# Optimization experiments

Measured on AMD Instinct MI355X. Metric: run time of the kernel, lower is better.

## Reference

```python
import jax, jax.numpy as jnp
import numpy as np

NEG_SLOPE = 0.2


def gat_layer(x, src, dst, W, a_src, a_dst, b, heads, out_c, concat):
    N = x.shape[0]
    h = (x @ W).reshape(N, heads, out_c)                      # [N,H,C]
    alpha_s = jnp.einsum('nhc,hc->nh', h, a_src)              # [N,H]
    alpha_d = jnp.einsum('nhc,hc->nh', h, a_dst)              # [N,H]
    e = jax.nn.leaky_relu(alpha_s[src] + alpha_d[dst], NEG_SLOPE)  # [E,H]
    # softmax over incoming edges per destination node (segment softmax)
    m = jax.ops.segment_max(e, dst, num_segments=N)
    m = jnp.where(jnp.isfinite(m), m, 0.0)
    ex = jnp.exp(e - m[dst])
    denom = jax.ops.segment_sum(ex, dst, num_segments=N)
    alpha = ex / (denom[dst] + 1e-16)                         # [E,H]
    out = jax.ops.segment_sum(alpha[:, :, None] * h[src], dst, num_segments=N)  # [N,H,C]
    out = out.reshape(N, heads * out_c) if concat else out.mean(axis=1)
    return out + b


def setup_inputs() -> dict:
    key = jax.random.key(0)
    ks = jax.random.split(key, 12)
    N, E, D, H, C, G = 20000, 160000, 256, 4, 128, 64
    x = jax.random.normal(ks[0], (N, D), dtype=jnp.float32)
    edge_index = jax.random.randint(ks[1], (2, E), 0, N)
    batch = jnp.sort(jax.random.randint(ks[2], (N,), 0, G))
    s = 0.05
    params = {
        'W1': jax.random.normal(ks[3], (D, H * C), jnp.float32) * s,
        'a_src1': jax.random.normal(ks[4], (H, C), jnp.float32) * s,
        'a_dst1': jax.random.normal(ks[5], (H, C), jnp.float32) * s,
        'b1': jnp.zeros((H * C,), jnp.float32),
        'W2': jax.random.normal(ks[6], (H * C, C), jnp.float32) * s,
        'a_src2': jax.random.normal(ks[7], (1, C), jnp.float32) * s,
        'a_dst2': jax.random.normal(ks[8], (1, C), jnp.float32) * s,
        'b2': jnp.zeros((C,), jnp.float32),
        'fc1_W': jax.random.normal(ks[9], (C, C // 2), jnp.float32) * s,
        'fc1_b': jnp.zeros((C // 2,), jnp.float32),
        'fc2_W': jax.random.normal(ks[10], (C // 2, 1), jnp.float32) * s,
        'fc2_b': jnp.zeros((1,), jnp.float32),
    }
    return dict(x=x, edge_index=edge_index, batch=batch, **params)


def reference(x, edge_index, batch, W1, a_src1, a_dst1, b1, W2, a_src2, a_dst2, b2,
              fc1_W, fc1_b, fc2_W, fc2_b):
    N = x.shape[0]
    G = 64  # number of graphs
    # add self-loops (PyG GATConv default)
    loop = jnp.arange(N, dtype=edge_index.dtype)
    src = jnp.concatenate([edge_index[0], loop])
    dst = jnp.concatenate([edge_index[1], loop])
    h = jax.nn.relu(gat_layer(x, src, dst, W1, a_src1, a_dst1, b1, 4, 128, True))
    h = gat_layer(h, src, dst, W2, a_src2, a_dst2, b2, 1, 128, False)
    # global mean pool per graph
    sums = jax.ops.segment_sum(h, batch, num_segments=G)
    cnts = jax.ops.segment_sum(jnp.ones((N,), h.dtype), batch, num_segments=G)
    pooled = sums / jnp.maximum(cnts, 1.0)[:, None]          # [G,128]
    out = jax.nn.relu(pooled @ fc1_W + fc1_b)
    return out @ fc2_W + fc2_b                                # [G,1]
```

## Files before the change

### kernel.cpp

```cpp
#include <hip/hip_runtime.h>
#include <hip/hip_bf16.h>
#include <cstdint>
#include <cstddef>

#define NEG_SLOPE 0.2f

typedef __attribute__((ext_vector_type(8))) __bf16 bf16x8;
typedef __attribute__((ext_vector_type(4))) __bf16 bf16x4;
typedef __attribute__((ext_vector_type(2))) __bf16 bf16x2;
typedef __attribute__((ext_vector_type(4))) float  f32x4;

__device__ __forceinline__ float lrelu(float v) {
    return (v < 0.f) ? NEG_SLOPE * v : v;
}

template<int MF, int NF, bool STORE_BF16>
__global__ __launch_bounds__(256) void gemm_mfma(
    const __bf16* __restrict__ A, const __bf16* __restrict__ Bt,
    void* __restrict__ Cout, int M, int N, int K)
{
    const int tid  = threadIdx.x;
    const int wave = tid >> 6, lane = tid & 63;
    const int wr = wave >> 1, wc = wave & 1;
    const int rowbase = blockIdx.y * (32 * MF) + wr * (16 * MF);
    const int colbase = blockIdx.x * (32 * NF) + wc * (16 * NF);
    const int l15 = lane & 15, kg = lane >> 4;

    size_t aoff[MF], boff[NF];
    #pragma unroll
    for (int mf = 0; mf < MF; ++mf) {
        int r = rowbase + mf * 16 + l15;
        if (r > M - 1) r = M - 1;
        aoff[mf] = (size_t)r * K + kg * 8;
    }
    #pragma unroll
    for (int nf = 0; nf < NF; ++nf) {
        int c = colbase + nf * 16 + l15;
        boff[nf] = (size_t)c * K + kg * 8;
    }

    f32x4 acc[MF][NF];
    #pragma unroll
    for (int mf = 0; mf < MF; ++mf)
        #pragma unroll
        for (int nf = 0; nf < NF; ++nf)
            acc[mf][nf] = (f32x4){0.f, 0.f, 0.f, 0.f};

    #pragma unroll 2
    for (int k0 = 0; k0 < K; k0 += 32) {
        bf16x8 af[MF], bfr[NF];
        #pragma unroll
        for (int mf = 0; mf < MF; ++mf)
            af[mf] = *(const bf16x8*)(A + aoff[mf] + k0);
        #pragma unroll
        for (int nf = 0; nf < NF; ++nf)
            bfr[nf] = *(const bf16x8*)(Bt + boff[nf] + k0);
        #pragma unroll
        for (int mf = 0; mf < MF; ++mf)
            #pragma unroll
            for (int nf = 0; nf < NF; ++nf)
                acc[mf][nf] = __builtin_amdgcn_mfma_f32_16x16x32_bf16(af[mf], bfr[nf], acc[mf][nf], 0, 0, 0);
    }

    #pragma unroll
    for (int mf = 0; mf < MF; ++mf)
        #pragma unroll
        for (int j = 0; j < 4; ++j) {
            int r = rowbase + mf * 16 + kg * 4 + j;
            if (r < M) {
                #pragma unroll
                for (int nf = 0; nf < NF; ++nf) {
                    int c = colbase + nf * 16 + l15;
                    if (STORE_BF16)
                        ((__bf16*)Cout)[(size_t)r * N + c] = (__bf16)acc[mf][nf][j];
                    else
                        ((float*)Cout)[(size_t)r * N + c] = acc[mf][nf][j];
                }
            }
        }
}

__global__ __launch_bounds__(256) void gemm1_agg(
    const __bf16* __restrict__ aggx,
    const __bf16* __restrict__ w1t,
    const float* __restrict__ b1, const float* __restrict__ wsd2,
    __bf16* __restrict__ out1b,
    float* __restrict__ ps_part, float* __restrict__ pd_part,
    int M)
{
    const int head = blockIdx.x;
    const int tid  = threadIdx.x;
    const int wave = tid >> 6, lane = tid & 63;
    const int wr = wave >> 1, wc = wave & 1;
    const int rowbase = blockIdx.y * 128 + wr * 64;
    const int l15 = lane & 15, kg = lane >> 4;

    size_t aoff[4], boff[4];
    #pragma unroll
    for (int mf = 0; mf < 4; ++mf) {
        int r = rowbase + mf * 16 + l15;
        if (r > M - 1) r = M - 1;
        aoff[mf] = (size_t)r * 1024 + head * 256 + kg * 8;
    }
    #pragma unroll
    for (int nf = 0; nf < 4; ++nf) {
        int c = head * 128 + wc * 64 + nf * 16 + l15;
        boff[nf] = (size_t)c * 256 + kg * 8;
    }

    f32x4 acc[4][4];
    #pragma unroll
    for (int mf = 0; mf < 4; ++mf)
        #pragma unroll
        for (int nf = 0; nf < 4; ++nf)
            acc[mf][nf] = (f32x4){0.f, 0.f, 0.f, 0.f};

    #pragma unroll 2
    for (int k0 = 0; k0 < 256; k0 += 32) {
        bf16x8 af[4], bfr[4];
        #pragma unroll
        for (int mf = 0; mf < 4; ++mf)
            af[mf] = *(const bf16x8*)(aggx + aoff[mf] + k0);
        #pragma unroll
        for (int nf = 0; nf < 4; ++nf)
            bfr[nf] = *(const bf16x8*)(w1t + boff[nf] + k0);
        #pragma unroll
        for (int mf = 0; mf < 4; ++mf)
            #pragma unroll
            for (int nf = 0; nf < 4; ++nf)
                acc[mf][nf] = __builtin_amdgcn_mfma_f32_16x16x32_bf16(af[mf], bfr[nf], acc[mf][nf], 0, 0, 0);
    }

    __shared__ float smp[2][128], smd[2][128];

    #pragma unroll
    for (int mf = 0; mf < 4; ++mf)
        #pragma unroll
        for (int j = 0; j < 4; ++j) {
            int r = rowbase + mf * 16 + kg * 4 + j;
            float ps = 0.f, pd = 0.f;
            #pragma unroll
            for (int nf = 0; nf < 4; ++nf) {
                int col = head * 128 + wc * 64 + nf * 16 + l15;
                float o = fmaxf(acc[mf][nf][j] + b1[col], 0.f);
                if (r < M)
                    out1b[(size_t)r * 512 + col] = (__bf16)o;
                ps = fmaf(o, wsd2[col], ps);
                pd = fmaf(o, wsd2[512 + col], pd);
            }
            #pragma unroll
            for (int t = 1; t < 16; t <<= 1) {
                ps += __shfl_xor(ps, t);
                pd += __shfl_xor(pd, t);
            }
            if (l15 == 0) {
                int lr = wr * 64 + mf * 16 + kg * 4 + j;
                smp[wc][lr] = ps;
                smd[wc][lr] = pd;
            }
        }
    __syncthreads();
    if (tid < 128) {
        int r = blockIdx.y * 128 + tid;
        if (r < M) {
            ps_part[(size_t)r * 4 + head] = smp[0][tid] + smp[1][tid];
            pd_part[(size_t)r * 4 + head] = smd[0][tid] + smd[1][tid];
        }
    }
}

__global__ void prep_kernel(const float* __restrict__ W1, const float* __restrict__ W2,
                            const float* __restrict__ as1w, const float* __restrict__ ad1w,
                            const float* __restrict__ as2w, const float* __restrict__ ad2w,
                            const int* __restrict__ batch,
                            __bf16* __restrict__ w1t, __bf16* __restrict__ w2t,
                            float* __restrict__ wsd1, float* __restrict__ wsd2,
                            int* __restrict__ gstart, int* __restrict__ cnt,
                            int N, int G)
{
    int t = blockIdx.x * 256 + threadIdx.x;
    if (t < 131072) {
        int i = t;
        int k = i >> 9, n = i & 511;
        w1t[n * 256 + k] = (__bf16)W1[i];
    } else if (t < 196608) {
        int j = t - 131072;
        int k = j >> 7, n = j & 127;
        w2t[n * 512 + k] = (__bf16)W2[j];
    } else if (t < 199680) {
        int t2 = t - 196608;
        if (t2 < 2048) {
            int k = t2 >> 3, v = t2 & 7, h = v >> 1;
            const float* av = (v & 1) ? (ad1w + h * 128) : (as1w + h * 128);
            float s = 0.f;
            for (int c = 0; c < 128; ++c) s += W1[k * 512 + h * 128 + c] * av[c];
            wsd1[v * 256 + k] = s;
        } else {
            int t3 = t2 - 2048;
            int k = t3 >> 1, v = t3 & 1;
            const float* av = v ? ad2w : as2w;
            float s = 0.f;
            for (int c = 0; c < 128; ++c) s += W2[k * 128 + c] * av[c];
            wsd2[v * 512 + k] = s;
        }
    } else if (t < 199680 + N) {
        int n = t - 199680;
        int b    = batch[n];
        int prev = (n == 0) ? -1 : batch[n - 1];
        for (int g = prev + 1; g <= b; ++g) gstart[g] = n;
        if (n == N - 1) {
            for (int g = b + 1; g <= G; ++g) gstart[g] = N;
        }
    } else if (t < 199680 + 2 * N) {
        cnt[t - 199680 - N] = 0;
    }
}

__global__ __launch_bounds__(256) void count_cvtx(
    const int* __restrict__ ei, int* __restrict__ cnt,
    const float* __restrict__ x, const float* __restrict__ wsd1,
    __bf16* __restrict__ xb, float* __restrict__ as1_, float* __restrict__ ad1_,
    int ET, int E0, int N, int CB)
{
    if ((int)blockIdx.x < CB) {
        int e = blockIdx.x * 256 + threadIdx.x;
        if (e >= ET) return;
        int d = (e < E0) ? ei[E0 + e] : (e - E0);
        atomicAdd(&cnt[d], 1);
        return;
    }
    int bid = blockIdx.x - CB;
    int wave = threadIdx.x >> 6, lane = threadIdx.x & 63;
    int n = bid * 4 + wave;
    if (n >= N) return;
    float4 xv = *(const float4*)&x[(size_t)n * 256 + lane * 4];
    bf16x4 xo;
    xo[0] = (__bf16)xv.x; xo[1] = (__bf16)xv.y; xo[2] = (__bf16)xv.z; xo[3] = (__bf16)xv.w;
    *(bf16x4*)&xb[(size_t)n * 256 + lane * 4] = xo;
    float p[8];
    #pragma unroll
    for (int v = 0; v < 8; ++v) {
        float4 wv = *(const float4*)&wsd1[v * 256 + lane * 4];
        p[v] = xv.x * wv.x + xv.y * wv.y + xv.z * wv.z + xv.w * wv.w;
    }
    #pragma unroll
    for (int v = 0; v < 8; ++v)
        #pragma unroll
        for (int s = 1; s < 64; s <<= 1) p[v] += __shfl_xor(p[v], s);
    if (lane == 0) {
        #pragma unroll
        for (int h = 0; h < 4; ++h) {
            as1_[n * 4 + h] = p[2 * h];
            ad1_[n * 4 + h] = p[2 * h + 1];
        }
    }
}

__global__ __launch_bounds__(1024) void scan_gmax(
    const int* __restrict__ cnt, int* __restrict__ offs, int* __restrict__ cur,
    const float* __restrict__ as1_, float* __restrict__ gmax1, int n)
{
    constexpr int CHUNK = 20;
    int t = threadIdx.x;
    int base = t * CHUNK;
    int v[CHUNK];
    int s = 0;
    #pragma unroll
    for (int i = 0; i < CHUNK; ++i) {
        int idx = base + i;
        int xv = (idx < n) ? cnt[idx] : 0;
        v[i] = s; s += xv;
    }
    int lane = t & 63, w = t >> 6;
    int sc = s;
    #pragma unroll
    for (int d = 1; d < 64; d <<= 1) {
        int o = __shfl_up(sc, d);
        if (lane >= d) sc += o;
    }
    __shared__ int wt[16], wb[17];
    __shared__ float gsm[16][4];
    if (lane == 63) wt[w] = sc;
    __syncthreads();
    if (t == 0) {
        int acc = 0;
        for (int i = 0; i < 16; ++i) { wb[i] = acc; acc += wt[i]; }
        wb[16] = acc;
    }
    __syncthreads();
    int ebase = wb[w] + (sc - s);
    #pragma unroll
    for (int i = 0; i < CHUNK; ++i) {
        int idx = base + i;
        if (idx < n) {
            int o = ebase + v[i];
            offs[idx] = o;
            cur[idx]  = o;
        }
    }
    if (t == 0) offs[n] = wb[16];

    float lm0 = -1e30f, lm1 = -1e30f, lm2 = -1e30f, lm3 = -1e30f;
    for (int i = t; i < n; i += 1024) {
        float4 a = *(const float4*)&as1_[(size_t)i * 4];
        lm0 = fmaxf(lm0, a.x); lm1 = fmaxf(lm1, a.y);
        lm2 = fmaxf(lm2, a.z); lm3 = fmaxf(lm3, a.w);
    }
    #pragma unroll
    for (int d = 1; d < 64; d <<= 1) {
        lm0 = fmaxf(lm0, __shfl_xor(lm0, d));
        lm1 = fmaxf(lm1, __shfl_xor(lm1, d));
        lm2 = fmaxf(lm2, __shfl_xor(lm2, d));
        lm3 = fmaxf(lm3, __shfl_xor(lm3, d));
    }
    if (lane == 0) {
        gsm[w][0] = lm0; gsm[w][1] = lm1; gsm[w][2] = lm2; gsm[w][3] = lm3;
    }
    __syncthreads();
    if (t == 0) {
        float m0 = -1e30f, m1 = -1e30f, m2 = -1e30f, m3 = -1e30f;
        for (int i = 0; i < 16; ++i) {
            m0 = fmaxf(m0, gsm[i][0]); m1 = fmaxf(m1, gsm[i][1]);
            m2 = fmaxf(m2, gsm[i][2]); m3 = fmaxf(m3, gsm[i][3]);
        }
        gmax1[0] = m0; gmax1[1] = m1; gmax1[2] = m2; gmax1[3] = m3;
    }
}

__global__ void scatter_kernel(const int* __restrict__ ei, int* __restrict__ cur,
                               int* __restrict__ eid, int ET, int E0)
{
    int e = blockIdx.x * blockDim.x + threadIdx.x;
    if (e >= ET) return;
    int d   = (e < E0) ? ei[E0 + e] : (e - E0);
    int pos = atomicAdd(&cur[d], 1);
    eid[pos] = e;
}

__global__ __launch_bounds__(256) void aggx_kernel(
    const __bf16* __restrict__ xb, const int* __restrict__ offs,
    const int* __restrict__ eid, const int* __restrict__ ei,
    const float* __restrict__ as1_, const float* __restrict__ ad1_,
    const float* __restrict__ gmax1,
    __bf16* __restrict__ aggx, int E0, int N)
{
    int wave = threadIdx.x >> 6, lane = threadIdx.x & 63;
    int n = blockIdx.x * 4 + wave;
    if (n >= N) return;
    int s0 = offs[n], s1 = offs[n + 1];
    float4 adv = *(const float4*)&ad1_[(size_t)n * 4];
    float m0 = lrelu(gmax1[0] + adv.x);
    float m1 = lrelu(gmax1[1] + adv.y);
    float m2 = lrelu(gmax1[2] + adv.z);
    float m3 = lrelu(gmax1[3] + adv.w);

    float d0 = 0.f, d1 = 0.f, d2 = 0.f, d3 = 0.f;
    float a0[4] = {0.f,0.f,0.f,0.f}, a1[4] = {0.f,0.f,0.f,0.f};
    float a2[4] = {0.f,0.f,0.f,0.f}, a3[4] = {0.f,0.f,0.f,0.f};
    const __bf16* xbase = xb + lane * 4;

    int j = s0;
    for (; j + 7 < s1; j += 8) {
        int s_[8]; float4 av_[8]; bf16x4 xv_[8];
        #pragma unroll
        for (int i = 0; i < 8; ++i) {
            int e = eid[j + i];
            s_[i] = (e < E0) ? ei[e] : (e - E0);
        }
        #pragma unroll
        for (int i = 0; i < 8; ++i) av_[i] = *(const float4*)&as1_[(size_t)s_[i] * 4];
        #pragma unroll
        for (int i = 0; i < 8; ++i) xv_[i] = *(const bf16x4*)(xbase + (size_t)s_[i] * 256);
        #pragma unroll
        for (int i = 0; i < 8; ++i) {
            float w0 = __expf(lrelu(av_[i].x + adv.x) - m0); d0 += w0;
            float w1 = __expf(lrelu(av_[i].y + adv.y) - m1); d1 += w1;
            float w2 = __expf(lrelu(av_[i].z + adv.z) - m2); d2 += w2;
            float w3 = __expf(lrelu(av_[i].w + adv.w) - m3); d3 += w3;
            float xf[4];
            #pragma unroll
            for (int c = 0; c < 4; ++c) xf[c] = (float)xv_[i][c];
            #pragma unroll
            for (int c = 0; c < 4; ++c) {
                a0[c] = fmaf(w0, xf[c], a0[c]);
                a1[c] = fmaf(w1, xf[c], a1[c]);
                a2[c] = fmaf(w2, xf[c], a2[c]);
                a3[c] = fmaf(w3, xf[c], a3[c]);
            }
        }
    }
    for (; j < s1; ++j) {
        int e = eid[j];
        int s = (e < E0) ? ei[e] : (e - E0);
        float4 av = *(const float4*)&as1_[(size_t)s * 4];
        bf16x4 xv = *(const bf16x4*)(xbase + (size_t)s * 256);
        float w0 = __expf(lrelu(av.x + adv.x) - m0); d0 += w0;
        float w1 = __expf(lrelu(av.y + adv.y) - m1); d1 += w1;
        float w2 = __expf(lrelu(av.z + adv.z) - m2); d2 += w2;
        float w3 = __expf(lrelu(av.w + adv.w) - m3); d3 += w3;
        float xf[4];
        #pragma unroll
        for (int c = 0; c < 4; ++c) xf[c] = (float)xv[c];
        #pragma unroll
        for (int c = 0; c < 4; ++c) {
            a0[c] = fmaf(w0, xf[c], a0[c]);
            a1[c] = fmaf(w1, xf[c], a1[c]);
            a2[c] = fmaf(w2, xf[c], a2[c]);
            a3[c] = fmaf(w3, xf[c], a3[c]);
        }
    }

    float i0 = 1.f / (d0 + 1e-16f);
    float i1 = 1.f / (d1 + 1e-16f);
    float i2 = 1.f / (d2 + 1e-16f);
    float i3 = 1.f / (d3 + 1e-16f);
    __bf16* obase = aggx + (size_t)n * 1024 + lane * 4;
    bf16x4 o;
    #pragma unroll
    for (int c = 0; c < 4; ++c) o[c] = (__bf16)(a0[c] * i0);
    *(bf16x4*)(obase + 0)   = o;
    #pragma unroll
    for (int c = 0; c < 4; ++c) o[c] = (__bf16)(a1[c] * i1);
    *(bf16x4*)(obase + 256) = o;
    #pragma unroll
    for (int c = 0; c < 4; ++c) o[c] = (__bf16)(a2[c] * i2);
    *(bf16x4*)(obase + 512) = o;
    #pragma unroll
    for (int c = 0; c < 4; ++c) o[c] = (__bf16)(a3[c] * i3);
    *(bf16x4*)(obase + 768) = o;
}

__global__ __launch_bounds__(256) void aggregate2_kernel(
    const __bf16* __restrict__ h2b, const int* __restrict__ offs,
    const int* __restrict__ eid, const int* __restrict__ ei,
    const float* __restrict__ ps_part, const float* __restrict__ pd_part,
    const float* __restrict__ b2, float* __restrict__ out2, int E0, int N)
{
    int wave = threadIdx.x >> 6, lane = threadIdx.x & 63;
    int n = blockIdx.x * 4 + wave;
    if (n >= N) return;
    int s0 = offs[n], s1 = offs[n + 1];
    float4 pdv = *(const float4*)&pd_part[(size_t)n * 4];
    float adn = (pdv.x + pdv.y) + (pdv.z + pdv.w);

    float m = -1e30f;
    for (int j = s0 + lane; j < s1; j += 64) {
        int e = eid[j];
        int s = (e < E0) ? ei[e] : (e - E0);
        float4 pv = *(const float4*)&ps_part[(size_t)s * 4];
        float v = lrelu(((pv.x + pv.y) + (pv.z + pv.w)) + adn);
        m = fmaxf(m, v);
    }
    #pragma unroll
    for (int t = 1; t < 64; t <<= 1) m = fmaxf(m, __shfl_xor(m, t));

    float den = 0.f;
    float c0 = 0.f, c1 = 0.f;
    const __bf16* hbase = h2b + lane * 2;
    int j = s0;
    for (; j + 7 < s1; j += 8) {
        int s_[8]; float4 pv_[8]; bf16x2 h_[8];
        #pragma unroll
        for (int i = 0; i < 8; ++i) {
            int e = eid[j + i];
            s_[i] = (e < E0) ? ei[e] : (e - E0);
        }
        #pragma unroll
        for (int i = 0; i < 8; ++i) pv_[i] = *(const float4*)&ps_part[(size_t)s_[i] * 4];
        #pragma unroll
        for (int i = 0; i < 8; ++i) h_[i] = *(const bf16x2*)(hbase + (size_t)s_[i] * 128);
        #pragma unroll
        for (int i = 0; i < 8; ++i) {
            float v = lrelu(((pv_[i].x + pv_[i].y) + (pv_[i].z + pv_[i].w)) + adn);
            float w = __expf(v - m);
            den += w;
            c0 = fmaf(w, (float)h_[i][0], c0);
            c1 = fmaf(w, (float)h_[i][1], c1);
        }
    }
    for (; j < s1; ++j) {
        int e = eid[j];
        int s = (e < E0) ? ei[e] : (e - E0);
        float4 pv = *(const float4*)&ps_part[(size_t)s * 4];
        float v = lrelu(((pv.x + pv.y) + (pv.z + pv.w)) + adn);
        float w = __expf(v - m);
        den += w;
        bf16x2 hv = *(const bf16x2*)(hbase + (size_t)s * 128);
        c0 = fmaf(w, (float)hv[0], c0);
        c1 = fmaf(w, (float)hv[1], c1);
    }
    float inv = 1.f / (den + 1e-16f);
    float2 o;
    o.x = c0 * inv + b2[lane * 2 + 0];
    o.y = c1 * inv + b2[lane * 2 + 1];
    *(float2*)&out2[(size_t)n * 128 + lane * 2] = o;
}

#define POOL_S 16
__global__ void pool_stage1(const float* __restrict__ out2, const int* __restrict__ gstart,
                            float* __restrict__ partial, int C)
{
    int g = blockIdx.x, slice = blockIdx.y;
    int c = threadIdx.x;
    int s = gstart[g], e = gstart[g + 1];
    int len = e - s;
    int chunk = (len + POOL_S - 1) / POOL_S;
    int n0 = s + slice * chunk;
    int n1 = min(n0 + chunk, e);
    float acc = 0.f;
    for (int n = n0; n < n1; ++n) acc += out2[(size_t)n * C + c];
    partial[((size_t)g * POOL_S + slice) * C + c] = acc;
}

__global__ __launch_bounds__(128) void pool_head(
    const float* __restrict__ partial, const int* __restrict__ gstart,
    const float* __restrict__ fc1W, const float* __restrict__ fc1b,
    const float* __restrict__ fc2W, const float* __restrict__ fc2b,
    float* __restrict__ out)
{
    int g = blockIdx.x;
    int t = threadIdx.x;
    __shared__ float pl[128];
    float acc = 0.f;
    #pragma unroll
    for (int s = 0; s < POOL_S; ++s)
        acc += partial[((size_t)g * POOL_S + s) * 128 + t];
    float cntf = (float)(gstart[g + 1] - gstart[g]);
    pl[t] = acc / fmaxf(cntf, 1.0f);
    __syncthreads();
    if (t < 64) {
        float v = 0.f;
        for (int c = 0; c < 128; ++c)
            v += pl[c] * fc1W[c * 64 + t];
        v = fmaxf(v + fc1b[t], 0.f) * fc2W[t];
        #pragma unroll
        for (int s = 32; s > 0; s >>= 1) v += __shfl_down(v, s);
        if (t == 0) out[g] = v + fc2b[0];
    }
}

extern "C" void kernel_launch(void* const* d_in, const int* in_sizes, int n_in,
                              void* d_out, int out_size, void* d_ws, size_t ws_size,
                              hipStream_t stream)
{
    const float* x    = (const float*)d_in[0];
    const int*   ei   = (const int*)d_in[1];
    const int*   batch= (const int*)d_in[2];
    const float* W1   = (const float*)d_in[3];
    const float* as1w = (const float*)d_in[4];
    const float* ad1w = (const float*)d_in[5];
    const float* b1   = (const float*)d_in[6];
    const float* W2   = (const float*)d_in[7];
    const float* as2w = (const float*)d_in[8];
    const float* ad2w = (const float*)d_in[9];
    const float* b2   = (const float*)d_in[10];
    const float* fc1W = (const float*)d_in[11];
    const float* fc1b = (const float*)d_in[12];
    const float* fc2W = (const float*)d_in[13];
    const float* fc2b = (const float*)d_in[14];
    float* out = (float*)d_out;

    const int D = 256, C = 128, G = 64;
    const int N  = in_sizes[0] / D;
    const int E0 = in_sizes[1] / 2;
    const int ET = E0 + N;

    char* p = (char*)d_ws;
    auto alloc = [&](size_t bytes) -> char* {
        char* r = p;
        p += (bytes + 255) & ~(size_t)255;
        return r;
    };
    __bf16* xb    = (__bf16*)alloc((size_t)N * D * 2);
    __bf16* aggx  = (__bf16*)alloc((size_t)N * 4 * 256 * 2);
    __bf16* out1b = (__bf16*)alloc((size_t)N * 512 * 2);
    __bf16* h2b   = (__bf16*)alloc((size_t)N * C * 2);
    float*  out2  = (float*)alloc((size_t)N * C * 4);
    __bf16* w1t   = (__bf16*)alloc((size_t)256 * 512 * 2);
    __bf16* w2t   = (__bf16*)alloc((size_t)512 * 128 * 2);
    float* wsd1   = (float*)alloc(8 * 256 * 4);
    float* wsd2   = (float*)alloc(2 * 512 * 4);
    float* gmax1  = (float*)alloc(4 * 4);
    float* as1_   = (float*)alloc((size_t)N * 4 * 4);
    float* ad1_   = (float*)alloc((size_t)N * 4 * 4);
    float* ps_part= (float*)alloc((size_t)N * 4 * 4);
    float* pd_part= (float*)alloc((size_t)N * 4 * 4);
    int*   cnt    = (int*)alloc((size_t)N * 4);
    int*   cur    = (int*)alloc((size_t)N * 4);
    int*   offs   = (int*)alloc((size_t)(N + 1) * 4);
    int*   eid    = (int*)alloc((size_t)ET * 4);
    int*   gstart = (int*)alloc((size_t)(G + 1) * 4);
    float* partial= (float*)alloc((size_t)G * POOL_S * C * 4);

    {
        int total = 199680 + 2 * N;
        prep_kernel<<<(total + 255) / 256, 256, 0, stream>>>(
            W1, W2, as1w, ad1w, as2w, ad2w, batch,
            w1t, w2t, wsd1, wsd2, gstart, cnt, N, G);
    }

    {
        int CB = (ET + 255) / 256;
        count_cvtx<<<CB + N / 4, 256, 0, stream>>>(
            ei, cnt, x, wsd1, xb, as1_, ad1_, ET, E0, N, CB);
    }

    scan_gmax<<<1, 1024, 0, stream>>>(cnt, offs, cur, as1_, gmax1, N);

    scatter_kernel<<<(ET + 255) / 256, 256, 0, stream>>>(ei, cur, eid, ET, E0);

    aggx_kernel<<<(N + 3) / 4, 256, 0, stream>>>(
        xb, offs, eid, ei, as1_, ad1_, gmax1, aggx, E0, N);

    gemm1_agg<<<dim3(4, (N + 127) / 128), 256, 0, stream>>>(
        aggx, w1t, b1, wsd2, out1b, ps_part, pd_part, N);

    gemm_mfma<2, 2, true><<<dim3(C / 64, (N + 63) / 64), 256, 0, stream>>>(
        out1b, w2t, h2b, N, C, 512);

    aggregate2_kernel<<<(N + 3) / 4, 256, 0, stream>>>(
        h2b, offs, eid, ei, ps_part, pd_part, b2, out2, E0, N);

    pool_stage1<<<dim3(G, POOL_S), C, 0, stream>>>(out2, gstart, partial, C);
    pool_head<<<G, 128, 0, stream>>>(partial, gstart, fc1W, fc1b, fc2W, fc2b, out);
}
```

Before: 222.1 us.

## Store source ids in CSR, precompute per-edge weights cooperatively, use global-max softmax bound

The scatter kernel now stores source node ids directly, which removes the eid-to-ei indirection in both aggregation kernels. In each aggregation, every lane computes one edge's softmax weight at once and stages it in shared memory, so weights are no longer recomputed redundantly by all 64 lanes. Layer 2 drops its per-node max pass in favour of a global max of alpha_src, found by a new kernel with an ordered-key atomicMax, plus precomputed scalar as2/ad2 arrays. A global upper bound for the shift risks exp underflow when scores are widely spread, and the shared memory is reused across chunks without an explicit wave barrier.

```diff
diff --git a/kernel.cpp b/kernel.cpp
--- a/kernel.cpp
+++ b/kernel.cpp
@@ -12,6 +12,15 @@
 
 __device__ __forceinline__ float lrelu(float v) {
     return (v < 0.f) ? NEG_SLOPE * v : v;
+}
+
+__device__ __forceinline__ unsigned fkey(float x) {
+    unsigned b = __float_as_uint(x);
+    return b ^ (unsigned)(((int)b >> 31) | 0x80000000);
+}
+__device__ __forceinline__ float funkey(unsigned k) {
+    unsigned b = (k & 0x80000000u) ? (k ^ 0x80000000u) : ~k;
+    return __uint_as_float(b);
 }
 
 template<int MF, int NF, bool STORE_BF16>
@@ -176,6 +185,7 @@
                             __bf16* __restrict__ w1t, __bf16* __restrict__ w2t,
                             float* __restrict__ wsd1, float* __restrict__ wsd2,
                             int* __restrict__ gstart, int* __restrict__ cnt,
+                            unsigned* __restrict__ gmax2u,
                             int N, int G)
 {
     int t = blockIdx.x * 256 + threadIdx.x;
@@ -213,6 +223,8 @@
         }
     } else if (t < 199680 + 2 * N) {
         cnt[t - 199680 - N] = 0;
+    } else if (t == 199680 + 2 * N) {
+        *gmax2u = fkey(-1e30f);
     }
 }
 
@@ -328,22 +340,25 @@
 }
 
 __global__ void scatter_kernel(const int* __restrict__ ei, int* __restrict__ cur,
-                               int* __restrict__ eid, int ET, int E0)
+                               int* __restrict__ srcs, int ET, int E0)
 {
     int e = blockIdx.x * blockDim.x + threadIdx.x;
     if (e >= ET) return;
-    int d   = (e < E0) ? ei[E0 + e] : (e - E0);
+    int d = (e < E0) ? ei[E0 + e] : (e - E0);
+    int s = (e < E0) ? ei[e] : (e - E0);
     int pos = atomicAdd(&cur[d], 1);
-    eid[pos] = e;
+    srcs[pos] = s;
 }
 
 __global__ __launch_bounds__(256) void aggx_kernel(
     const __bf16* __restrict__ xb, const int* __restrict__ offs,
-    const int* __restrict__ eid, const int* __restrict__ ei,
+    const int* __restrict__ srcs,
     const float* __restrict__ as1_, const float* __restrict__ ad1_,
     const float* __restrict__ gmax1,
-    __bf16* __restrict__ aggx, int E0, int N)
-{
+    __bf16* __restrict__ aggx, int N)
+{
+    __shared__ float w4s[4][64][4];
+    __shared__ int   sidx[4][64];
     int wave = threadIdx.x >> 6, lane = threadIdx.x & 63;
     int n = blockIdx.x * 4 + wave;
     if (n >= N) return;
@@ -359,55 +374,68 @@
     float a2[4] = {0.f,0.f,0.f,0.f}, a3[4] = {0.f,0.f,0.f,0.f};
     const __bf16* xbase = xb + lane * 4;
 
-    int j = s0;
-    for (; j + 7 < s1; j += 8) {
-        int s_[8]; float4 av_[8]; bf16x4 xv_[8];
-        #pragma unroll
-        for (int i = 0; i < 8; ++i) {
-            int e = eid[j + i];
-            s_[i] = (e < E0) ? ei[e] : (e - E0);
-        }
-        #pragma unroll
-        for (int i = 0; i < 8; ++i) av_[i] = *(const float4*)&as1_[(size_t)s_[i] * 4];
-        #pragma unroll
-        for (int i = 0; i < 8; ++i) xv_[i] = *(const bf16x4*)(xbase + (size_t)s_[i] * 256);
-        #pragma unroll
-        for (int i = 0; i < 8; ++i) {
-            float w0 = __expf(lrelu(av_[i].x + adv.x) - m0); d0 += w0;
-            float w1 = __expf(lrelu(av_[i].y + adv.y) - m1); d1 += w1;
-            float w2 = __expf(lrelu(av_[i].z + adv.z) - m2); d2 += w2;
-            float w3 = __expf(lrelu(av_[i].w + adv.w) - m3); d3 += w3;
+    for (int base = s0; base < s1; base += 64) {
+        int cnt = min(64, s1 - base);
+        if (lane < cnt) {
+            int s = srcs[base + lane];
+            float4 av = *(const float4*)&as1_[(size_t)s * 4];
+            float w0 = __expf(lrelu(av.x + adv.x) - m0);
+            float w1 = __expf(lrelu(av.y + adv.y) - m1);
+            float w2 = __expf(lrelu(av.z + adv.z) - m2);
+            float w3 = __expf(lrelu(av.w + adv.w) - m3);
+            d0 += w0; d1 += w1; d2 += w2; d3 += w3;
+            sidx[wave][lane] = s;
+            w4s[wave][lane][0] = w0; w4s[wave][lane][1] = w1;
+            w4s[wave][lane][2] = w2; w4s[wave][lane][3] = w3;
+        }
+        int j = 0;
+        for (; j + 7 < cnt; j += 8) {
+            int s_[8]; float4 w_[8]; bf16x4 xv_[8];
+            #pragma unroll
+            for (int i = 0; i < 8; ++i) {
+                s_[i] = sidx[wave][j + i];
+                w_[i] = *(const float4*)&w4s[wave][j + i][0];
+            }
+            #pragma unroll
+            for (int i = 0; i < 8; ++i)
+                xv_[i] = *(const bf16x4*)(xbase + (size_t)s_[i] * 256);
+            #pragma unroll
+            for (int i = 0; i < 8; ++i) {
+                float xf[4];
+                #pragma unroll
+                for (int c = 0; c < 4; ++c) xf[c] = (float)xv_[i][c];
+                #pragma unroll
+                for (int c = 0; c < 4; ++c) {
+                    a0[c] = fmaf(w_[i].x, xf[c], a0[c]);
+                    a1[c] = fmaf(w_[i].y, xf[c], a1[c]);
+                    a2[c] = fmaf(w_[i].z, xf[c], a2[c]);
+                    a3[c] = fmaf(w_[i].w, xf[c], a3[c]);
+                }
+            }
+        }
+        for (; j < cnt; ++j) {
+            int s = sidx[wave][j];
+            float4 w = *(const float4*)&w4s[wave][j][0];
+            bf16x4 xv = *(const bf16x4*)(xbase + (size_t)s * 256);
             float xf[4];
             #pragma unroll
-            for (int c = 0; c < 4; ++c) xf[c] = (float)xv_[i][c];
+            for (int c = 0; c < 4; ++c) xf[c] = (float)xv[c];
             #pragma unroll
             for (int c = 0; c < 4; ++c) {
-                a0[c] = fmaf(w0, xf[c], a0[c]);
-                a1[c] = fmaf(w1, xf[c], a1[c]);
-                a2[c] = fmaf(w2, xf[c], a2[c]);
-                a3[c] = fmaf(w3, xf[c], a3[c]);
-            }
-        }
-    }
-    for (; j < s1; ++j) {
-        int e = eid[j];
-        int s = (e < E0) ? ei[e] : (e - E0);
-        float4 av = *(const float4*)&as1_[(size_t)s * 4];
-        bf16x4 xv = *(const bf16x4*)(xbase + (size_t)s * 256);
-        float w0 = __expf(lrelu(av.x + adv.x) - m0); d0 += w0;
-        float w1 = __expf(lrelu(av.y + adv.y) - m1); d1 += w1;
-        float w2 = __expf(lrelu(av.z + adv.z) - m2); d2 += w2;
-        float w3 = __expf(lrelu(av.w + adv.w) - m3); d3 += w3;
-        float xf[4];
-        #pragma unroll
-        for (int c = 0; c < 4; ++c) xf[c] = (float)xv[c];
-        #pragma unroll
-        for (int c = 0; c < 4; ++c) {
-            a0[c] = fmaf(w0, xf[c], a0[c]);
-            a1[c] = fmaf(w1, xf[c], a1[c]);
-            a2[c] = fmaf(w2, xf[c], a2[c]);
-            a3[c] = fmaf(w3, xf[c], a3[c]);
-        }
+                a0[c] = fmaf(w.x, xf[c], a0[c]);
+                a1[c] = fmaf(w.y, xf[c], a1[c]);
+                a2[c] = fmaf(w.z, xf[c], a2[c]);
+                a3[c] = fmaf(w.w, xf[c], a3[c]);
+            }
+        }
+    }
+
+    #pragma unroll
+    for (int t = 1; t < 64; t <<= 1) {
+        d0 += __shfl_xor(d0, t);
+        d1 += __shfl_xor(d1, t);
+        d2 += __shfl_xor(d2, t);
+        d3 += __shfl_xor(d3, t);
     }
 
     float i0 = 1.f / (d0 + 1e-16f);
@@ -430,65 +458,84 @@
     *(bf16x4*)(obase + 768) = o;
 }
 
+__global__ __launch_bounds__(256) void sum2_kernel(
+    const float* __restrict__ ps_part, const float* __restrict__ pd_part,
+    float* __restrict__ as2, float* __restrict__ ad2,
+    unsigned* __restrict__ gmax2u, int N)
+{
+    int i = blockIdx.x * 256 + threadIdx.x;
+    float lm = -1e30f;
+    if (i < N) {
+        float4 p = *(const float4*)&ps_part[(size_t)i * 4];
+        float4 q = *(const float4*)&pd_part[(size_t)i * 4];
+        float s = (p.x + p.y) + (p.z + p.w);
+        float d = (q.x + q.y) + (q.z + q.w);
+        as2[i] = s;
+        ad2[i] = d;
+        lm = s;
+    }
+    #pragma unroll
+    for (int t = 1; t < 64; t <<= 1) lm = fmaxf(lm, __shfl_xor(lm, t));
+    if ((threadIdx.x & 63) == 0) atomicMax(gmax2u, fkey(lm));
+}
+
 __global__ __launch_bounds__(256) void aggregate2_kernel(
     const __bf16* __restrict__ h2b, const int* __restrict__ offs,
-    const int* __restrict__ eid, const int* __restrict__ ei,
-    const float* __restrict__ ps_part, const float* __restrict__ pd_part,
-    const float* __restrict__ b2, float* __restrict__ out2, int E0, int N)
-{
+    const int* __restrict__ srcs,
+    const float* __restrict__ as2, const float* __restrict__ ad2,
+    const unsigned* __restrict__ gmax2u,
+    const float* __restrict__ b2, float* __restrict__ out2, int N)
+{
+    __shared__ float wls[4][64];
+    __shared__ int   sidx[4][64];
     int wave = threadIdx.x >> 6, lane = threadIdx.x & 63;
     int n = blockIdx.x * 4 + wave;
     if (n >= N) return;
     int s0 = offs[n], s1 = offs[n + 1];
-    float4 pdv = *(const float4*)&pd_part[(size_t)n * 4];
-    float adn = (pdv.x + pdv.y) + (pdv.z + pdv.w);
-
-    float m = -1e30f;
-    for (int j = s0 + lane; j < s1; j += 64) {
-        int e = eid[j];
-        int s = (e < E0) ? ei[e] : (e - E0);
-        float4 pv = *(const float4*)&ps_part[(size_t)s * 4];
-        float v = lrelu(((pv.x + pv.y) + (pv.z + pv.w)) + adn);
-        m = fmaxf(m, v);
-    }
-    #pragma unroll
-    for (int t = 1; t < 64; t <<= 1) m = fmaxf(m, __shfl_xor(m, t));
+    float adn = ad2[n];
+    float m = lrelu(funkey(*gmax2u) + adn);
 
     float den = 0.f;
     float c0 = 0.f, c1 = 0.f;
     const __bf16* hbase = h2b + lane * 2;
-    int j = s0;
-    for (; j + 7 < s1; j += 8) {
-        int s_[8]; float4 pv_[8]; bf16x2 h_[8];
-        #pragma unroll
-        for (int i = 0; i < 8; ++i) {
-            int e = eid[j + i];
-            s_[i] = (e < E0) ? ei[e] : (e - E0);
-        }
-        #pragma unroll
-        for (int i = 0; i < 8; ++i) pv_[i] = *(const float4*)&ps_part[(size_t)s_[i] * 4];
-        #pragma unroll
-        for (int i = 0; i < 8; ++i) h_[i] = *(const bf16x2*)(hbase + (size_t)s_[i] * 128);
-        #pragma unroll
-        for (int i = 0; i < 8; ++i) {
-            float v = lrelu(((pv_[i].x + pv_[i].y) + (pv_[i].z + pv_[i].w)) + adn);
-            float w = __expf(v - m);
+
+    for (int base = s0; base < s1; base += 64) {
+        int cnt = min(64, s1 - base);
+        if (lane < cnt) {
+            int s = srcs[base + lane];
+            float w = __expf(lrelu(as2[s] + adn) - m);
             den += w;
-            c0 = fmaf(w, (float)h_[i][0], c0);
-            c1 = fmaf(w, (float)h_[i][1], c1);
-        }
-    }
-    for (; j < s1; ++j) {
-        int e = eid[j];
-        int s = (e < E0) ? ei[e] : (e - E0);
-        float4 pv = *(const float4*)&ps_part[(size_t)s * 4];
-        float v = lrelu(((pv.x + pv.y) + (pv.z + pv.w)) + adn);
-        float w = __expf(v - m);
-        den += w;
-        bf16x2 hv = *(const bf16x2*)(hbase + (size_t)s * 128);
-        c0 = fmaf(w, (float)hv[0], c0);
-        c1 = fmaf(w, (float)hv[1], c1);
-    }
+            sidx[wave][lane] = s;
+            wls[wave][lane]  = w;
+        }
+        int j = 0;
+        for (; j + 7 < cnt; j += 8) {
+            int s_[8]; float w_[8]; bf16x2 h_[8];
+            #pragma unroll
+            for (int i = 0; i < 8; ++i) {
+                s_[i] = sidx[wave][j + i];
+                w_[i] = wls[wave][j + i];
+            }
+            #pragma unroll
+            for (int i = 0; i < 8; ++i)
+                h_[i] = *(const bf16x2*)(hbase + (size_t)s_[i] * 128);
+            #pragma unroll
+            for (int i = 0; i < 8; ++i) {
+                c0 = fmaf(w_[i], (float)h_[i][0], c0);
+                c1 = fmaf(w_[i], (float)h_[i][1], c1);
+            }
+        }
+        for (; j < cnt; ++j) {
+            int s = sidx[wave][j];
+            float w = wls[wave][j];
+            bf16x2 hv = *(const bf16x2*)(hbase + (size_t)s * 128);
+            c0 = fmaf(w, (float)hv[0], c0);
+            c1 = fmaf(w, (float)hv[1], c1);
+        }
+    }
+
+    #pragma unroll
+    for (int t = 1; t < 64; t <<= 1) den += __shfl_xor(den, t);
     float inv = 1.f / (den + 1e-16f);
     float2 o;
     o.x = c0 * inv + b2[lane * 2 + 0];
@@ -581,22 +628,25 @@
     float* wsd1   = (float*)alloc(8 * 256 * 4);
     float* wsd2   = (float*)alloc(2 * 512 * 4);
     float* gmax1  = (float*)alloc(4 * 4);
+    unsigned* gmax2u = (unsigned*)alloc(4);
     float* as1_   = (float*)alloc((size_t)N * 4 * 4);
     float* ad1_   = (float*)alloc((size_t)N * 4 * 4);
     float* ps_part= (float*)alloc((size_t)N * 4 * 4);
     float* pd_part= (float*)alloc((size_t)N * 4 * 4);
+    float* as2    = (float*)alloc((size_t)N * 4);
+    float* ad2    = (float*)alloc((size_t)N * 4);
     int*   cnt    = (int*)alloc((size_t)N * 4);
     int*   cur    = (int*)alloc((size_t)N * 4);
     int*   offs   = (int*)alloc((size_t)(N + 1) * 4);
-    int*   eid    = (int*)alloc((size_t)ET * 4);
+    int*   srcs   = (int*)alloc((size_t)ET * 4);
     int*   gstart = (int*)alloc((size_t)(G + 1) * 4);
     float* partial= (float*)alloc((size_t)G * POOL_S * C * 4);
 
     {
-        int total = 199680 + 2 * N;
+        int total = 199680 + 2 * N + 1;
         prep_kernel<<<(total + 255) / 256, 256, 0, stream>>>(
             W1, W2, as1w, ad1w, as2w, ad2w, batch,
-            w1t, w2t, wsd1, wsd2, gstart, cnt, N, G);
+            w1t, w2t, wsd1, wsd2, gstart, cnt, gmax2u, N, G);
     }
 
     {
@@ -607,19 +657,22 @@
 
     scan_gmax<<<1, 1024, 0, stream>>>(cnt, offs, cur, as1_, gmax1, N);
 
-    scatter_kernel<<<(ET + 255) / 256, 256, 0, stream>>>(ei, cur, eid, ET, E0);
+    scatter_kernel<<<(ET + 255) / 256, 256, 0, stream>>>(ei, cur, srcs, ET, E0);
 
     aggx_kernel<<<(N + 3) / 4, 256, 0, stream>>>(
-        xb, offs, eid, ei, as1_, ad1_, gmax1, aggx, E0, N);
+        xb, offs, srcs, as1_, ad1_, gmax1, aggx, N);
 
     gemm1_agg<<<dim3(4, (N + 127) / 128), 256, 0, stream>>>(
         aggx, w1t, b1, wsd2, out1b, ps_part, pd_part, N);
 
+    sum2_kernel<<<(N + 255) / 256, 256, 0, stream>>>(
+        ps_part, pd_part, as2, ad2, gmax2u, N);
+
     gemm_mfma<2, 2, true><<<dim3(C / 64, (N + 63) / 64), 256, 0, stream>>>(
         out1b, w2t, h2b, N, C, 512);
 
     aggregate2_kernel<<<(N + 3) / 4, 256, 0, stream>>>(
-        h2b, offs, eid, ei, ps_part, pd_part, b2, out2, E0, N);
+        h2b, offs, srcs, as2, ad2, gmax2u, b2, out2, N);
 
     pool_stage1<<<dim3(G, POOL_S), C, 0, stream>>>(out2, gstart, partial, C);
     pool_head<<<G, 128, 0, stream>>>(partial, gstart, fc1W, fc1b, fc2W, fc2b, out);
```

New measurement: 200.2 us. 9.9% less time.
